# Kernel optimization log

Hardware: AMD Instinct MI355X
Metric: run time of the kernel (lower is better)

The kernel has to match this reference:

```python
import jax, jax.numpy as jnp
import numpy as np

C = 128
N_NODES = 50000
N_EDGES = 800000
BN_EPS = 1e-5


def batchnorm(h, w, b):
    # BatchNorm1d in training mode: normalize with batch mean and biased variance.
    mu = jnp.mean(h, axis=0)
    var = jnp.mean((h - mu) ** 2, axis=0)
    return (h - mu) * jax.lax.rsqrt(var + BN_EPS) * w + b


def setup_inputs() -> dict:
    key = jax.random.key(0)
    ks = jax.random.split(key, 10)
    lim1 = 1.0 / np.sqrt(2 * C)
    lim2 = 1.0 / np.sqrt(2 * C)
    return {
        "x": jax.random.normal(ks[0], (N_NODES, C), dtype=jnp.float32),
        "edge_index": jax.random.randint(ks[1], (2, N_EDGES), 0, N_NODES),
        "edge_attr": jax.random.normal(ks[2], (N_EDGES, C), dtype=jnp.float32),
        "u": jax.random.normal(ks[3], (256, C), dtype=jnp.float32),
        "batch": jax.random.randint(ks[4], (N_NODES,), 0, 256),
        "w1": jax.random.uniform(ks[5], (C, 2 * C), jnp.float32, -lim1, lim1),
        "b1": jax.random.uniform(ks[6], (C,), jnp.float32, -lim1, lim1),
        "bn1_w": jnp.ones((C,), jnp.float32),
        "bn1_b": jnp.zeros((C,), jnp.float32),
        "w2": jax.random.uniform(ks[7], (C, 2 * C), jnp.float32, -lim2, lim2),
        "b2": jax.random.uniform(ks[8], (C,), jnp.float32, -lim2, lim2),
        "bn2_w": jnp.ones((C,), jnp.float32),
        "bn2_b": jnp.zeros((C,), jnp.float32),
    }


def reference(x, edge_index, edge_attr, u, batch,
              w1, b1, bn1_w, bn1_b, w2, b2, bn2_w, bn2_b):
    row, col = edge_index[0], edge_index[1]
    n = x.shape[0]
    # edge MLP: cat([x[row], edge_attr]) -> Linear -> BN -> ELU
    h = jnp.concatenate([x[row], edge_attr], axis=1)  # [E, 2C]
    h = h @ w1.T + b1
    h = jax.nn.elu(batchnorm(h, bn1_w, bn1_b))
    # scatter_mean over destination nodes (empty segments -> 0)
    s = jax.ops.segment_sum(h, col, num_segments=n)
    cnt = jax.ops.segment_sum(jnp.ones((h.shape[0],), h.dtype), col, num_segments=n)
    agg = s / jnp.maximum(cnt, 1.0)[:, None]
    # node MLP: cat([x, agg]) -> Linear -> BN -> ELU
    out = jnp.concatenate([x, agg], axis=1) @ w2.T + b2
    return jax.nn.elu(batchnorm(out, bn2_w, bn2_b))
```

## Files before the change

kernel.cpp:

```cpp
#include <hip/hip_runtime.h>

typedef _Float16 f16;
typedef __attribute__((ext_vector_type(8))) _Float16 f16x8;
typedef __attribute__((ext_vector_type(4))) _Float16 f16x4;
typedef __attribute__((ext_vector_type(2))) _Float16 f16x2;
typedef __attribute__((ext_vector_type(4))) float f32x4;

#define CC 128
#define K2 256
#define BN_EPS 1e-5f

__device__ __forceinline__ float elu(float v) {
    return v > 0.f ? v : __expf(v) - 1.f;
}

__global__ __launch_bounds__(256)
void edge_gemm(const float* __restrict__ x, const int* __restrict__ rowidx,
               const float* __restrict__ eattr, const float* __restrict__ w1,
               const float* __restrict__ b1,
               f16* __restrict__ hbuf, float* __restrict__ sum1,
               float* __restrict__ sq1, int E, int nTiles)
{
    __shared__ __align__(16) f16 a_lds[32 * 264];
    __shared__ __align__(16) f16 h_lds[32 * 136];
    __shared__ int rows_s[32];

    const int tid  = threadIdx.x;
    const int lane = tid & 63;
    const int wave = tid >> 6;
    const int quad = lane >> 4;
    const int l16  = lane & 15;
    const int n_off = wave * 32;

    f16x8 bfrag[8][2];
    float bias[2];
    #pragma unroll
    for (int ns = 0; ns < 2; ++ns) {
        int n = n_off + ns * 16 + l16;
        bias[ns] = b1[n];
        #pragma unroll
        for (int kk = 0; kk < 8; ++kk) {
            const float* wr = w1 + n * K2 + kk * 32 + quad * 8;
            f16x8 f;
            #pragma unroll
            for (int j = 0; j < 8; ++j) f[j] = (f16)wr[j];
            bfrag[kk][ns] = f;
        }
    }

    float st_s[2] = {0.f, 0.f};
    float st_q[2] = {0.f, 0.f};
    const f32x4 zero4 = {0.f, 0.f, 0.f, 0.f};

    for (int t = blockIdx.x; t < nTiles; t += gridDim.x) {
        const int e0 = t * 32;
        if (tid < 32) rows_s[tid] = (e0 + tid < E) ? rowidx[e0 + tid] : 0;
        __syncthreads();

        #pragma unroll
        for (int i = 0; i < 8; ++i) {
            int chunk = tid + i * 256;
            int r  = chunk >> 6;
            int cc = (chunk & 63) * 4;
            float4 v = {0.f, 0.f, 0.f, 0.f};
            if (e0 + r < E) {
                const float* src = (cc < CC)
                    ? x + (size_t)rows_s[r] * CC + cc
                    : eattr + (size_t)(e0 + r) * CC + (cc - CC);
                v = *(const float4*)src;
            }
            f16 tmp[4] = {(f16)v.x, (f16)v.y, (f16)v.z, (f16)v.w};
            *(f16x4*)&a_lds[r * 264 + cc] = *(f16x4*)tmp;
        }
        __syncthreads();

        f32x4 acc[2][2];
        acc[0][0] = zero4; acc[0][1] = zero4; acc[1][0] = zero4; acc[1][1] = zero4;

        #pragma unroll
        for (int kk = 0; kk < 8; ++kk) {
            int kb = kk * 32 + quad * 8;
            f16x8 af0 = *(f16x8*)&a_lds[l16 * 264 + kb];
            f16x8 af1 = *(f16x8*)&a_lds[(16 + l16) * 264 + kb];
            acc[0][0] = __builtin_amdgcn_mfma_f32_16x16x32_f16(af0, bfrag[kk][0], acc[0][0], 0, 0, 0);
            acc[0][1] = __builtin_amdgcn_mfma_f32_16x16x32_f16(af0, bfrag[kk][1], acc[0][1], 0, 0, 0);
            acc[1][0] = __builtin_amdgcn_mfma_f32_16x16x32_f16(af1, bfrag[kk][0], acc[1][0], 0, 0, 0);
            acc[1][1] = __builtin_amdgcn_mfma_f32_16x16x32_f16(af1, bfrag[kk][1], acc[1][1], 0, 0, 0);
        }

        #pragma unroll
        for (int ms = 0; ms < 2; ++ms) {
            #pragma unroll
            for (int ns = 0; ns < 2; ++ns) {
                int col = n_off + ns * 16 + l16;
                #pragma unroll
                for (int r = 0; r < 4; ++r) {
                    int rl = ms * 16 + quad * 4 + r;
                    float v = acc[ms][ns][r] + bias[ns];
                    if (e0 + rl < E) { st_s[ns] += v; st_q[ns] += v * v; }
                    h_lds[rl * 136 + col] = (f16)v;
                }
            }
        }
        __syncthreads();

        #pragma unroll
        for (int j = 0; j < 2; ++j) {
            int chunk = tid + j * 256;
            int r  = chunk >> 4;
            int cc = (chunk & 15) * 8;
            if (e0 + r < E) {
                f16x8 v = *(f16x8*)&h_lds[r * 136 + cc];
                *(f16x8*)&hbuf[(size_t)(e0 + r) * CC + cc] = v;
            }
        }
    }

    #pragma unroll
    for (int ns = 0; ns < 2; ++ns) {
        float s = st_s[ns], q = st_q[ns];
        s += __shfl_xor(s, 16, 64); q += __shfl_xor(q, 16, 64);
        s += __shfl_xor(s, 32, 64); q += __shfl_xor(q, 32, 64);
        if (lane < 16) {
            int c = n_off + ns * 16 + lane;
            atomicAdd(&sum1[c], s);
            atomicAdd(&sq1[c], q);
        }
    }
}

__global__ void finalize_stats(const float* __restrict__ sum, const float* __restrict__ sq,
                               const float* __restrict__ bnw, const float* __restrict__ bnb,
                               float* __restrict__ scale, float* __restrict__ shift,
                               float invN)
{
    int c = threadIdx.x;
    float mu  = sum[c] * invN;
    float var = sq[c] * invN - mu * mu;
    float sc  = bnw[c] * rsqrtf(var + BN_EPS);
    scale[c] = sc;
    shift[c] = bnb[c] - mu * sc;
}

__global__ __launch_bounds__(256)
void k_hist(const int* __restrict__ colidx, int* __restrict__ cnt_i, int E)
{
    int e = blockIdx.x * 256 + threadIdx.x;
    if (e < E) atomicAdd(&cnt_i[colidx[e]], 1);
}

__global__ __launch_bounds__(1024)
void k_scan(const int* __restrict__ cnt_i, int* __restrict__ start,
            int* __restrict__ cursor, int Nn)
{
    __shared__ int wsum[16];
    const int tid  = threadIdx.x;
    const int lane = tid & 63;
    const int wid  = tid >> 6;
    int carry = 0;
    const int nChunks = (Nn + 1023) / 1024;
    for (int c = 0; c < nChunks; ++c) {
        int i = c * 1024 + tid;
        int v = (i < Nn) ? cnt_i[i] : 0;
        int s = v;
        #pragma unroll
        for (int off = 1; off < 64; off <<= 1) {
            int t = __shfl_up(s, off, 64);
            if (lane >= off) s += t;
        }
        if (lane == 63) wsum[wid] = s;
        __syncthreads();
        if (tid < 16) {
            int si = wsum[tid];
            #pragma unroll
            for (int off = 1; off < 16; off <<= 1) {
                int t = __shfl_up(si, off, 64);
                if (tid >= off) si += t;
            }
            wsum[tid] = si;
        }
        __syncthreads();
        int base = carry + (wid > 0 ? wsum[wid - 1] : 0);
        int excl = base + s - v;
        if (i < Nn) { start[i] = excl; cursor[i] = excl; }
        int total = wsum[15];
        __syncthreads();
        carry += total;
    }
    if (tid == 0) start[Nn] = carry;
}

__global__ __launch_bounds__(256)
void k_fill(const int* __restrict__ colidx, int* __restrict__ cursor,
            int* __restrict__ elist, int E)
{
    int e = blockIdx.x * 256 + threadIdx.x;
    if (e < E) {
        int p = atomicAdd(&cursor[colidx[e]], 1);
        elist[p] = e;
    }
}

__global__ __launch_bounds__(256)
void gather_nodes(const f16* __restrict__ hbuf, const int* __restrict__ start,
                  const int* __restrict__ elist,
                  const float* __restrict__ scale, const float* __restrict__ shift,
                  f16* __restrict__ agg, int Nn)
{
    const int tid  = threadIdx.x;
    const int lane = tid & 63;
    const int wave = tid >> 6;
    const int node = blockIdx.x * 4 + wave;
    if (node >= Nn) return;

    const float sc0 = scale[2 * lane],  sc1 = scale[2 * lane + 1];
    const float sh0 = shift[2 * lane],  sh1 = shift[2 * lane + 1];
    const int s0 = start[node], s1 = start[node + 1];
    float a0 = 0.f, a1 = 0.f;

    for (int base = s0; base < s1; base += 64) {
        int e_l = (base + lane < s1) ? elist[base + lane] : 0;
        int m = s1 - base; if (m > 64) m = 64;
        for (int j = 0; j < m; j += 4) {
            f16x2 hv[4];
            #pragma unroll
            for (int k = 0; k < 4; ++k) {
                int jj = j + k; if (jj > m - 1) jj = m - 1;
                int e = __shfl(e_l, jj, 64);
                hv[k] = *(const f16x2*)&hbuf[(size_t)e * CC + 2 * lane];
            }
            #pragma unroll
            for (int k = 0; k < 4; ++k) {
                if (j + k < m) {
                    a0 += elu((float)hv[k].x * sc0 + sh0);
                    a1 += elu((float)hv[k].y * sc1 + sh1);
                }
            }
        }
    }
    const int deg = s1 - s0;
    const float inv = deg > 0 ? 1.f / (float)deg : 0.f;
    f16x2 o; o.x = (f16)(a0 * inv); o.y = (f16)(a1 * inv);
    *(f16x2*)&agg[(size_t)node * CC + 2 * lane] = o;
}

__global__ __launch_bounds__(256)
void node_gemm(const float* __restrict__ x, const f16* __restrict__ agg,
               const float* __restrict__ w2, const float* __restrict__ b2,
               float* __restrict__ outp, float* __restrict__ sum2,
               float* __restrict__ sq2, int Nn, int nTiles)
{
    __shared__ __align__(16) f16 a_lds[32 * 264];
    __shared__ __align__(16) float f_lds[32 * 132];

    const int tid  = threadIdx.x;
    const int lane = tid & 63;
    const int wave = tid >> 6;
    const int quad = lane >> 4;
    const int l16  = lane & 15;
    const int n_off = wave * 32;

    f16x8 bfrag[8][2];
    float bias[2];
    #pragma unroll
    for (int ns = 0; ns < 2; ++ns) {
        int n = n_off + ns * 16 + l16;
        bias[ns] = b2[n];
        #pragma unroll
        for (int kk = 0; kk < 8; ++kk) {
            const float* wr = w2 + n * K2 + kk * 32 + quad * 8;
            f16x8 f;
            #pragma unroll
            for (int j = 0; j < 8; ++j) f[j] = (f16)wr[j];
            bfrag[kk][ns] = f;
        }
    }

    float st_s[2] = {0.f, 0.f};
    float st_q[2] = {0.f, 0.f};
    const f32x4 zero4 = {0.f, 0.f, 0.f, 0.f};

    for (int t = blockIdx.x; t < nTiles; t += gridDim.x) {
        const int i0 = t * 32;
        __syncthreads();

        #pragma unroll
        for (int i = 0; i < 8; ++i) {
            int chunk = tid + i * 256;
            int r  = chunk >> 6;
            int cc = (chunk & 63) * 4;
            int node = i0 + r;
            f16 tmp[4] = {(f16)0.f, (f16)0.f, (f16)0.f, (f16)0.f};
            if (node < Nn) {
                if (cc < CC) {
                    float4 v = *(const float4*)(x + (size_t)node * CC + cc);
                    tmp[0] = (f16)v.x; tmp[1] = (f16)v.y; tmp[2] = (f16)v.z; tmp[3] = (f16)v.w;
                } else {
                    *(f16x4*)tmp = *(const f16x4*)(agg + (size_t)node * CC + (cc - CC));
                }
            }
            *(f16x4*)&a_lds[r * 264 + cc] = *(f16x4*)tmp;
        }
        __syncthreads();

        f32x4 acc[2][2];
        acc[0][0] = zero4; acc[0][1] = zero4; acc[1][0] = zero4; acc[1][1] = zero4;

        #pragma unroll
        for (int kk = 0; kk < 8; ++kk) {
            int kb = kk * 32 + quad * 8;
            f16x8 af0 = *(f16x8*)&a_lds[l16 * 264 + kb];
            f16x8 af1 = *(f16x8*)&a_lds[(16 + l16) * 264 + kb];
            acc[0][0] = __builtin_amdgcn_mfma_f32_16x16x32_f16(af0, bfrag[kk][0], acc[0][0], 0, 0, 0);
            acc[0][1] = __builtin_amdgcn_mfma_f32_16x16x32_f16(af0, bfrag[kk][1], acc[0][1], 0, 0, 0);
            acc[1][0] = __builtin_amdgcn_mfma_f32_16x16x32_f16(af1, bfrag[kk][0], acc[1][0], 0, 0, 0);
            acc[1][1] = __builtin_amdgcn_mfma_f32_16x16x32_f16(af1, bfrag[kk][1], acc[1][1], 0, 0, 0);
        }

        #pragma unroll
        for (int ms = 0; ms < 2; ++ms) {
            #pragma unroll
            for (int ns = 0; ns < 2; ++ns) {
                int col = n_off + ns * 16 + l16;
                #pragma unroll
                for (int r = 0; r < 4; ++r) {
                    int rl = ms * 16 + quad * 4 + r;
                    float v = acc[ms][ns][r] + bias[ns];
                    if (i0 + rl < Nn) { st_s[ns] += v; st_q[ns] += v * v; }
                    f_lds[rl * 132 + col] = v;
                }
            }
        }
        __syncthreads();

        #pragma unroll
        for (int j = 0; j < 4; ++j) {
            int chunk = tid + j * 256;
            int r  = chunk >> 5;
            int cc = (chunk & 31) * 4;
            if (i0 + r < Nn) {
                float4 v = *(float4*)&f_lds[r * 132 + cc];
                *(float4*)&outp[(size_t)(i0 + r) * CC + cc] = v;
            }
        }
    }

    #pragma unroll
    for (int ns = 0; ns < 2; ++ns) {
        float s = st_s[ns], q = st_q[ns];
        s += __shfl_xor(s, 16, 64); q += __shfl_xor(q, 16, 64);
        s += __shfl_xor(s, 32, 64); q += __shfl_xor(q, 32, 64);
        if (lane < 16) {
            int c = n_off + ns * 16 + lane;
            atomicAdd(&sum2[c], s);
            atomicAdd(&sq2[c], q);
        }
    }
}

__global__ __launch_bounds__(256)
void bn_elu_out(float* __restrict__ out, const float* __restrict__ scale,
                const float* __restrict__ shift, int total4)
{
    int g = blockIdx.x * 256 + threadIdx.x;
    if (g >= total4) return;
    int cb = (g & 31) * 4;
    float4 v = ((const float4*)out)[g];
    v.x = elu(v.x * scale[cb + 0] + shift[cb + 0]);
    v.y = elu(v.y * scale[cb + 1] + shift[cb + 1]);
    v.z = elu(v.z * scale[cb + 2] + shift[cb + 2]);
    v.w = elu(v.w * scale[cb + 3] + shift[cb + 3]);
    ((float4*)out)[g] = v;
}

extern "C" void kernel_launch(void* const* d_in, const int* in_sizes, int n_in,
                              void* d_out, int out_size, void* d_ws, size_t ws_size,
                              hipStream_t stream)
{
    const float* x     = (const float*)d_in[0];
    const int*   eidx  = (const int*)d_in[1];
    const float* eattr = (const float*)d_in[2];
    const float* w1   = (const float*)d_in[5];
    const float* b1   = (const float*)d_in[6];
    const float* bn1w = (const float*)d_in[7];
    const float* bn1b = (const float*)d_in[8];
    const float* w2   = (const float*)d_in[9];
    const float* b2   = (const float*)d_in[10];
    const float* bn2w = (const float*)d_in[11];
    const float* bn2b = (const float*)d_in[12];

    const int Nn = in_sizes[0] / CC;
    const int E  = in_sizes[1] / 2;
    const int* rowi = eidx;
    const int* coli = eidx + E;

    char* ws = (char*)d_ws;
    size_t off = 0;
    f16* hbuf = (f16*)(ws + off);   off += (size_t)E * CC * sizeof(f16);
    f16* agg  = (f16*)(ws + off);   off += (size_t)Nn * CC * sizeof(f16);
    int* elist  = (int*)(ws + off); off += (size_t)E * sizeof(int);
    int* cnt_i  = (int*)(ws + off); off += (size_t)Nn * sizeof(int);
    int* start  = (int*)(ws + off); off += (size_t)(Nn + 1) * sizeof(int);
    int* cursor = (int*)(ws + off); off += (size_t)Nn * sizeof(int);
    float* sum1 = (float*)(ws + off);
    float* sq1  = sum1 + CC;
    float* sc1  = sum1 + 2 * CC;
    float* sh1  = sum1 + 3 * CC;
    float* sum2 = sum1 + 4 * CC;
    float* sq2  = sum1 + 5 * CC;
    float* sc2  = sum1 + 6 * CC;
    float* sh2  = sum1 + 7 * CC;

    hipMemsetAsync(cnt_i, 0, (size_t)Nn * sizeof(int), stream);
    hipMemsetAsync(sum1, 0, 8 * CC * sizeof(float), stream);

    const int nBe = (E + 255) / 256;
    k_hist<<<nBe, 256, 0, stream>>>(coli, cnt_i, E);
    k_scan<<<1, 1024, 0, stream>>>(cnt_i, start, cursor, Nn);
    k_fill<<<nBe, 256, 0, stream>>>(coli, cursor, elist, E);

    const int nT1 = (E + 31) / 32;
    edge_gemm<<<1024, 256, 0, stream>>>(x, rowi, eattr, w1, b1, hbuf, sum1, sq1, E, nT1);
    finalize_stats<<<1, CC, 0, stream>>>(sum1, sq1, bn1w, bn1b, sc1, sh1, 1.f / (float)E);

    gather_nodes<<<(Nn + 3) / 4, 256, 0, stream>>>(hbuf, start, elist, sc1, sh1, agg, Nn);

    const int nT2 = (Nn + 31) / 32;
    node_gemm<<<nT2, 256, 0, stream>>>(x, agg, w2, b2, (float*)d_out, sum2, sq2, Nn, nT2);
    finalize_stats<<<1, CC, 0, stream>>>(sum2, sq2, bn2w, bn2b, sc2, sh2, 1.f / (float)Nn);

    const int t4 = Nn * CC / 4;
    bn_elu_out<<<(t4 + 255) / 256, 256, 0, stream>>>((float*)d_out, sc2, sh2, t4);
}
```

Measured before the change: 1.110 ms.

## Prefetch next edge tile into registers and widen gather loads to f16x4

The edge GEMM now loads the next tile's gathered x rows and edge attributes into registers while the MFMA work on the current tile runs. This removes the shared-memory row-index staging and one barrier per tile, at the cost of a trailing barrier and more register pressure; launch bounds and grid size are raised to keep occupancy. The node gather kernel has each half-wave handle alternate edges with 4-channel f16x4 loads and combines the halves with a cross-lane shuffle. This halves the number of edge iterations per wave and issues wider memory accesses.

```diff
diff --git a/kernel.cpp b/kernel.cpp
--- a/kernel.cpp
+++ b/kernel.cpp
@@ -14,7 +14,7 @@
     return v > 0.f ? v : __expf(v) - 1.f;
 }
 
-__global__ __launch_bounds__(256)
+__global__ __launch_bounds__(256, 3)
 void edge_gemm(const float* __restrict__ x, const int* __restrict__ rowidx,
                const float* __restrict__ eattr, const float* __restrict__ w1,
                const float* __restrict__ b1,
@@ -23,7 +23,6 @@
 {
     __shared__ __align__(16) f16 a_lds[32 * 264];
     __shared__ __align__(16) f16 h_lds[32 * 136];
-    __shared__ int rows_s[32];
 
     const int tid  = threadIdx.x;
     const int lane = tid & 63;
@@ -31,6 +30,7 @@
     const int quad = lane >> 4;
     const int l16  = lane & 15;
     const int n_off = wave * 32;
+    const bool is_x = lane < 32;
 
     f16x8 bfrag[8][2];
     float bias[2];
@@ -52,27 +52,44 @@
     float st_q[2] = {0.f, 0.f};
     const f32x4 zero4 = {0.f, 0.f, 0.f, 0.f};
 
-    for (int t = blockIdx.x; t < nTiles; t += gridDim.x) {
+    float4 pre[8];
+
+    auto issue_prefetch = [&](int t) {
         const int e0 = t * 32;
-        if (tid < 32) rows_s[tid] = (e0 + tid < E) ? rowidx[e0 + tid] : 0;
-        __syncthreads();
-
+        int ridx[8];
         #pragma unroll
         for (int i = 0; i < 8; ++i) {
-            int chunk = tid + i * 256;
-            int r  = chunk >> 6;
-            int cc = (chunk & 63) * 4;
-            float4 v = {0.f, 0.f, 0.f, 0.f};
-            if (e0 + r < E) {
-                const float* src = (cc < CC)
-                    ? x + (size_t)rows_s[r] * CC + cc
-                    : eattr + (size_t)(e0 + r) * CC + (cc - CC);
-                v = *(const float4*)src;
-            }
-            f16 tmp[4] = {(f16)v.x, (f16)v.y, (f16)v.z, (f16)v.w};
-            *(f16x4*)&a_lds[r * 264 + cc] = *(f16x4*)tmp;
-        }
-        __syncthreads();
+            int e = e0 + wave + i * 4;
+            if (e > E - 1) e = E - 1;
+            ridx[i] = rowidx[e];
+        }
+        #pragma unroll
+        for (int i = 0; i < 8; ++i) {
+            int e = e0 + wave + i * 4;
+            if (e > E - 1) e = E - 1;
+            const float* src = is_x
+                ? x + (size_t)ridx[i] * CC + lane * 4
+                : eattr + (size_t)e * CC + (lane * 4 - CC);
+            pre[i] = *(const float4*)src;
+        }
+    };
+
+    int t0 = blockIdx.x;
+    if (t0 < nTiles) issue_prefetch(t0);
+
+    for (int t = t0; t < nTiles; t += gridDim.x) {
+        const int e0 = t * 32;
+
+        #pragma unroll
+        for (int i = 0; i < 8; ++i) {
+            int r = wave + i * 4;
+            f16 tmp[4] = {(f16)pre[i].x, (f16)pre[i].y, (f16)pre[i].z, (f16)pre[i].w};
+            *(f16x4*)&a_lds[r * 264 + lane * 4] = *(f16x4*)tmp;
+        }
+        __syncthreads();
+
+        int tn = t + gridDim.x;
+        if (tn < nTiles) issue_prefetch(tn);
 
         f32x4 acc[2][2];
         acc[0][0] = zero4; acc[0][1] = zero4; acc[1][0] = zero4; acc[1][1] = zero4;
@@ -114,6 +131,7 @@
                 *(f16x8*)&hbuf[(size_t)(e0 + r) * CC + cc] = v;
             }
         }
+        __syncthreads();
     }
 
     #pragma unroll
@@ -213,35 +231,50 @@
     const int node = blockIdx.x * 4 + wave;
     if (node >= Nn) return;
 
-    const float sc0 = scale[2 * lane],  sc1 = scale[2 * lane + 1];
-    const float sh0 = shift[2 * lane],  sh1 = shift[2 * lane + 1];
+    const int half = lane >> 5;
+    const int cb   = (lane & 31) * 4;
+
+    float sc[4], sh[4];
+    #pragma unroll
+    for (int c = 0; c < 4; ++c) { sc[c] = scale[cb + c]; sh[c] = shift[cb + c]; }
+
     const int s0 = start[node], s1 = start[node + 1];
-    float a0 = 0.f, a1 = 0.f;
+    float a[4] = {0.f, 0.f, 0.f, 0.f};
 
     for (int base = s0; base < s1; base += 64) {
-        int e_l = (base + lane < s1) ? elist[base + lane] : 0;
         int m = s1 - base; if (m > 64) m = 64;
-        for (int j = 0; j < m; j += 4) {
-            f16x2 hv[4];
+        int e_l = elist[base + (lane < m ? lane : m - 1)];
+        for (int j = 0; j < m; j += 8) {
+            f16x4 hv[4];
+            float va[4];
             #pragma unroll
             for (int k = 0; k < 4; ++k) {
-                int jj = j + k; if (jj > m - 1) jj = m - 1;
-                int e = __shfl(e_l, jj, 64);
-                hv[k] = *(const f16x2*)&hbuf[(size_t)e * CC + 2 * lane];
+                int idx = j + 2 * k + half;
+                va[k] = (idx < m) ? 1.f : 0.f;
+                int ii = (idx < m) ? idx : m - 1;
+                int e = __shfl(e_l, ii, 64);
+                hv[k] = *(const f16x4*)&hbuf[(size_t)e * CC + cb];
             }
             #pragma unroll
             for (int k = 0; k < 4; ++k) {
-                if (j + k < m) {
-                    a0 += elu((float)hv[k].x * sc0 + sh0);
-                    a1 += elu((float)hv[k].y * sc1 + sh1);
-                }
-            }
-        }
-    }
-    const int deg = s1 - s0;
-    const float inv = deg > 0 ? 1.f / (float)deg : 0.f;
-    f16x2 o; o.x = (f16)(a0 * inv); o.y = (f16)(a1 * inv);
-    *(f16x2*)&agg[(size_t)node * CC + 2 * lane] = o;
+                #pragma unroll
+                for (int c = 0; c < 4; ++c)
+                    a[c] += va[k] * elu((float)hv[k][c] * sc[c] + sh[c]);
+            }
+        }
+    }
+
+    #pragma unroll
+    for (int c = 0; c < 4; ++c) a[c] += __shfl_xor(a[c], 32, 64);
+
+    if (half == 0) {
+        const int deg = s1 - s0;
+        const float inv = deg > 0 ? 1.f / (float)deg : 0.f;
+        f16x4 o;
+        #pragma unroll
+        for (int c = 0; c < 4; ++c) o[c] = (f16)(a[c] * inv);
+        *(f16x4*)&agg[(size_t)node * CC + cb] = o;
+    }
 }
 
 __global__ __launch_bounds__(256)
@@ -420,7 +453,7 @@
     k_fill<<<nBe, 256, 0, stream>>>(coli, cursor, elist, E);
 
     const int nT1 = (E + 31) / 32;
-    edge_gemm<<<1024, 256, 0, stream>>>(x, rowi, eattr, w1, b1, hbuf, sum1, sq1, E, nT1);
+    edge_gemm<<<2048, 256, 0, stream>>>(x, rowi, eattr, w1, b1, hbuf, sum1, sq1, E, nT1);
     finalize_stats<<<1, CC, 0, stream>>>(sum1, sq1, bn1w, bn1b, sc1, sh1, 1.f / (float)E);
 
     gather_nodes<<<(Nn + 3) / 4, 256, 0, stream>>>(hbuf, start, elist, sc1, sh1, agg, Nn);
```

New measurement: 969.4 us. -12.6%, faster.
